# Kernel optimization log

Measured on AMD Instinct MI355X. Metric: run time of the kernel, lower is better.

Reference implementation:

```python
import jax, jax.numpy as jnp
import numpy as np

# uniform-size batching: B graphs, NC compound atoms, NP pocket residues each
B, NC, NP, H = 16, 64, 384, 128
CFEAT, PFEAT = 56, 1280
SCALE = 5.0  # coordinate_scale
LN_EPS = 1e-5


def setup_inputs() -> dict:
    key = jax.random.key(0)
    ks = jax.random.split(key, 16)
    inp = {
        "compound_feats": jax.random.normal(ks[0], (B * NC, CFEAT), jnp.float32),
        "pocket_feats": jax.random.normal(ks[1], (B * NP, PFEAT), jnp.float32),
        "complex_coords": jax.random.normal(ks[2], (B, 2 + NC + NP, 3), jnp.float32) * 10.0,
        "pocket_xyz": jax.random.normal(ks[3], (B, NP, 3), jnp.float32) * 10.0,
        "dis_map": jax.random.uniform(ks[4], (B * NP * NC,), jnp.float32) * 10.0,
        # learned parameters (xavier with gain=0.001 as in the torch init)
        "Wc": jax.random.normal(ks[5], (CFEAT, H), jnp.float32) * 0.001,
        "bc": jnp.zeros((H,), jnp.float32),
        "Wp": jax.random.normal(ks[6], (PFEAT, H), jnp.float32) * 0.001,
        "bp": jnp.zeros((H,), jnp.float32),
        "ln_g": jnp.ones((H,), jnp.float32),
        "ln_b": jnp.zeros((H,), jnp.float32),
        "W1": jax.random.normal(ks[7], (H, H), jnp.float32) * 0.001,
        "b1": jnp.zeros((H,), jnp.float32),
        "W2": jax.random.normal(ks[8], (H, 1), jnp.float32) * 0.001,
        "b2": jnp.zeros((1,), jnp.float32),
    }
    return inp


def _layernorm(x, g, b):
    m = jnp.mean(x, axis=-1, keepdims=True)
    v = jnp.mean(jnp.square(x - m), axis=-1, keepdims=True)
    return (x - m) * jax.lax.rsqrt(v + LN_EPS) * g + b


def reference(compound_feats, pocket_feats, complex_coords, pocket_xyz, dis_map,
              Wc, bc, Wp, bp, ln_g, ln_b, W1, b1, W2, b2):
    norm = lambda x: x / SCALE
    # input linears, then dense-batch (uniform sizes -> exact reshape)
    comp_emb = (compound_feats @ Wc + bc).reshape(B, NC, H)   # [B,NC,H]
    pock_emb = (pocket_feats @ Wp + bp).reshape(B, NP, H)     # [B,NP,H]
    # complex layout per graph: [glb_c, compound (NC), glb_p, pocket (NP)]
    # complex_binding_model treated as identity (see notes): emb/coords pass through.
    comp_coords_out = norm(complex_coords[:, 1:1 + NC])       # [B,NC,3] (normalized)
    pock_coords = norm(pocket_xyz)                            # [B,NP,3]
    # torch.cdist(pocket, compound): [B,NP,NC]
    diff = pock_coords[:, :, None, :] - comp_coords_out[:, None, :, :]
    pc_dis = jnp.sqrt(jnp.sum(jnp.square(diff), axis=-1))
    # layernorm + pairwise outer product + distmap MLP
    p_ln = _layernorm(pock_emb, ln_g, ln_b)
    c_ln = _layernorm(comp_emb, ln_g, ln_b)
    z = jnp.einsum('bik,bjk->bijk', p_ln, c_ln)               # [B,NP,NC,H]
    h = jax.nn.relu(z @ W1 + b1)
    b_logit = (h @ W2 + b2)[..., 0]                            # [B,NP,NC]
    # uniform sizes -> all-true masks, boolean-select is a flatten
    dis_map_pred_by_pair = jax.nn.sigmoid(b_logit.reshape(-1)) * 10.0
    dis_map_pred_by_coord = jnp.clip(pc_dis.reshape(-1) * SCALE, 0.0, 10.0)
    compound_coord_pred = (comp_coords_out * SCALE).reshape(B * NC, 3)
    compound_batch = jnp.repeat(jnp.arange(B, dtype=jnp.int32), NC)
    return (compound_coord_pred, compound_batch, dis_map_pred_by_pair,
            dis_map_pred_by_coord, dis_map)
```

## Files before the change

### kernel.cpp

```cpp
#include <hip/hip_runtime.h>
#include <hip/hip_bf16.h>

#define BB 16
#define NC 64
#define NP 384
#define HH 128
#define CF 56
#define PFT 1280

typedef float f32x4 __attribute__((ext_vector_type(4)));
typedef __bf16 bf16x8 __attribute__((ext_vector_type(8)));
typedef unsigned short u16x8 __attribute__((ext_vector_type(8)));
typedef unsigned short u16x4 __attribute__((ext_vector_type(4)));

static __device__ __forceinline__ unsigned short f2bfu(float f){
  __bf16 h = (__bf16)f;
  return __builtin_bit_cast(unsigned short, h);
}
static __device__ __forceinline__ float bfu2f(unsigned short u){
  __bf16 h = __builtin_bit_cast(__bf16, u);
  return (float)h;
}

__global__ __launch_bounds__(256) void k_prep(
    const float* __restrict__ cf, const float* __restrict__ Wc,
    const float* __restrict__ bc, const float* __restrict__ lng,
    const float* __restrict__ lnb, const float* __restrict__ Wp,
    const float* __restrict__ W1, const float* __restrict__ cc,
    const float* __restrict__ px, const float* __restrict__ dm,
    unsigned short* __restrict__ c_ln, unsigned short* __restrict__ wpt,
    unsigned short* __restrict__ w1t,
    float* __restrict__ out1, float* __restrict__ out4, float* __restrict__ out5){
  __shared__ unsigned short t[128][72];
  __shared__ float redc[2][2], redc2[2][2];
  int bx = blockIdx.x;
  int tid = threadIdx.x;
  if (bx < 20){
    int k0 = bx*64;
    #pragma unroll
    for (int i=0;i<8;i++){
      int fi = tid + i*256;
      int k  = fi>>5;
      int c4 = (fi&31)*4;
      float4 v = *(const float4*)(Wp + (size_t)(k0+k)*HH + c4);
      t[c4+0][k]=f2bfu(v.x); t[c4+1][k]=f2bfu(v.y);
      t[c4+2][k]=f2bfu(v.z); t[c4+3][k]=f2bfu(v.w);
    }
    __syncthreads();
    #pragma unroll
    for (int i=0;i<4;i++){
      int ci = tid + i*256;
      int col = ci>>3, kb = ci&7;
      u16x8 v = *(const u16x8*)&t[col][kb*8];
      *(u16x8*)(wpt + (size_t)col*PFT + k0 + kb*8) = v;
    }
  } else if (bx < 84){
    int idx = (bx-20)*256+tid;
    int k = idx>>7, m = idx&127;
    w1t[m*HH+k] = f2bfu(W1[idx]);
  } else if (bx < 596){
    int rh = tid>>7, m = tid&127;
    int row = (bx-84)*2 + rh;
    const float* cr = cf + row*CF;
    float acc = bc[m];
    #pragma unroll
    for (int k=0;k<CF;k++) acc += cr[k]*Wc[k*HH+m];
    float s=acc, s2=acc*acc;
    #pragma unroll
    for (int off=1; off<64; off<<=1){ s += __shfl_xor(s,off,64); s2 += __shfl_xor(s2,off,64); }
    int wid = (tid>>6)&1;
    if ((m&63)==0){ redc[rh][wid]=s; redc2[rh][wid]=s2; }
    __syncthreads();
    float S=redc[rh][0]+redc[rh][1], S2=redc2[rh][0]+redc2[rh][1];
    float mean = S*(1.0f/HH);
    float var  = S2*(1.0f/HH) - mean*mean;
    float rs = rsqrtf(var + 1e-5f);
    c_ln[(size_t)row*HH+m] = f2bfu((acc-mean)*rs*lng[m] + lnb[m]);
  } else if (bx < 608){
    int idx = (bx-596)*256+tid;
    if (idx < BB*NC*3){
      int bb = idx/(NC*3), rem = idx%(NC*3);
      float v = cc[(size_t)bb*(2+NC+NP)*3 + 3 + rem];
      out1[idx] = (v/5.0f)*5.0f;
    }
    if (idx < BB*NC) out1[BB*NC*3+idx] = (float)(idx>>6);
  } else {
    int idx = (bx-608)*256+tid;
    int b = idx/(NP*NC), r = idx%(NP*NC), i = r>>6, j = r&63;
    const float* pp = px + ((size_t)b*NP+i)*3;
    const float* cp = cc + (size_t)b*(2+NC+NP)*3 + 3 + (size_t)j*3;
    float dx=pp[0]/5.0f-cp[0]/5.0f;
    float dy=pp[1]/5.0f-cp[1]/5.0f;
    float dz=pp[2]/5.0f-cp[2]/5.0f;
    float d = sqrtf(dx*dx+dy*dy+dz*dz)*5.0f;
    d = fminf(fmaxf(d,0.f),10.f);
    out4[idx]=d;
    out5[idx]=dm[idx];
  }
}

__global__ __launch_bounds__(256) void k_main(
    const float* __restrict__ pf, const unsigned short* __restrict__ wpt,
    const float* __restrict__ bp, const float* __restrict__ lng,
    const float* __restrict__ lnb,
    const unsigned short* __restrict__ c_ln, const unsigned short* __restrict__ w1t,
    const float* __restrict__ b1, const float* __restrict__ W2,
    const float* __restrict__ b2p, float* __restrict__ out3){
  __shared__ __align__(16) unsigned short sA[2][16*64];
  __shared__ __align__(16) unsigned short sB[2][HH*64];
  __shared__ __align__(16) float sPf[12*HH];
  int tid = threadIdx.x;
  int w = tid>>6, lane = tid&63, q = lane&15, gr = lane>>4;
  int bx = blockIdx.x;
  int b  = bx>>5;
  int i0 = (bx&31)*12;
  size_t prow0 = (size_t)(b*NP + i0);
  *(unsigned short*)((char*)&sA[0][0] + 1536 + tid*2) = 0;
  *(unsigned short*)((char*)&sA[1][0] + 1536 + tid*2) = 0;
  f32x4 acc2[2];
  acc2[0]=(f32x4){0.f,0.f,0.f,0.f}; acc2[1]=(f32x4){0.f,0.f,0.f,0.f};
  int arow = tid>>4, ak4 = (tid&15)*4;
  float4 ra; u16x8 rb[4];
  #define LOADS1(KS) {                                                         \
    int kbase = (KS)*64;                                                       \
    if (arow < 12)                                                             \
      ra = *(const float4*)(pf + (prow0+arow)*PFT + kbase + ak4);              \
    _Pragma("unroll")                                                          \
    for (int i=0;i<4;i++){                                                     \
      int bi = tid + 256*i;                                                    \
      int col = bi>>3, kb = bi&7;                                              \
      rb[i] = *(const u16x8*)(wpt + (size_t)col*PFT + kbase + kb*8);           \
    }                                                                          \
  }
  #define WRITES1(BUF) {                                                       \
    char* A = (char*)&sA[BUF][0];                                              \
    char* Bc = (char*)&sB[BUF][0];                                             \
    if (arow < 12){                                                            \
      u16x4 h = { f2bfu(ra.x), f2bfu(ra.y), f2bfu(ra.z), f2bfu(ra.w) };        \
      *(u16x4*)(A + arow*128 + (((ak4>>3)^(arow&7))<<4) + ((ak4&7)<<1)) = h;   \
    }                                                                          \
    _Pragma("unroll")                                                          \
    for (int i=0;i<4;i++){                                                     \
      int bi = tid + 256*i;                                                    \
      int col = bi>>3, kb = bi&7;                                              \
      *(u16x8*)(Bc + col*128 + ((kb^(col&7))<<4)) = rb[i];                     \
    }                                                                          \
  }
  LOADS1(0)
  WRITES1(0)
  int cur = 0;
  for (int ks=0; ks<20; ks++){
    if (ks<19) LOADS1(ks+1)
    __syncthreads();
    char* A = (char*)&sA[cur][0];
    char* Bc = (char*)&sB[cur][0];
    #pragma unroll
    for (int kk=0;kk<2;kk++){
      bf16x8 a = *(bf16x8*)(A + q*128 + (((kk*4+gr)^(q&7))<<4));
      #pragma unroll
      for (int ct=0;ct<2;ct++){
        int col = w*32 + ct*16 + q;
        bf16x8 bfr = *(bf16x8*)(Bc + col*128 + (((kk*4+gr)^(col&7))<<4));
        acc2[ct] = __builtin_amdgcn_mfma_f32_16x16x32_bf16(a,bfr,acc2[ct],0,0,0);
      }
    }
    if (ks<19){ WRITES1(cur^1) cur ^= 1; }
  }
  __syncthreads();
  #pragma unroll
  for (int ct=0;ct<2;ct++){
    int col = w*32 + ct*16 + q;
    float bpv = bp[col];
    #pragma unroll
    for (int r=0;r<4;r++){
      int row = gr*4+r;
      if (row < 12) sPf[row*HH + col] = acc2[ct][r] + bpv;
    }
  }
  int jh = w&1, mh = w>>1;
  int j0 = jh*32, m0 = mh*64;
  u16x8 cfrag[2][4];
  #pragma unroll
  for (int jt=0;jt<2;jt++){
    const unsigned short* cb = c_ln + ((size_t)b*NC + j0 + jt*16 + q)*HH + gr*8;
    #pragma unroll
    for (int kt=0;kt<4;kt++) cfrag[jt][kt] = *(const u16x8*)(cb + kt*32);
  }
  u16x8 w1f[4][4];
  #pragma unroll
  for (int kt=0;kt<4;kt++)
    #pragma unroll
    for (int nt=0;nt<4;nt++)
      w1f[kt][nt] = *(const u16x8*)(w1t + (size_t)(m0+nt*16+q)*HH + kt*32 + gr*8);
  float b1v[4], w2v[4];
  #pragma unroll
  for (int nt=0;nt<4;nt++){ b1v[nt]=b1[m0+nt*16+q]; w2v[nt]=W2[m0+nt*16+q]; }
  float b2 = b2p[0];
  float* psumh = (float*)&sB[0][0];
  __syncthreads();
  {
    float g0 = lng[lane], g1 = lng[lane+64];
    float B0 = lnb[lane], B1 = lnb[lane+64];
    #pragma unroll
    for (int rr=0; rr<3; rr++){
      int row = w*3+rr;
      float a0 = sPf[row*HH + lane], a1 = sPf[row*HH + lane + 64];
      float s = a0+a1, s2 = a0*a0 + a1*a1;
      #pragma unroll
      for (int off=1; off<64; off<<=1){ s += __shfl_xor(s,off,64); s2 += __shfl_xor(s2,off,64); }
      float mean = s*(1.0f/HH);
      float var  = s2*(1.0f/HH) - mean*mean;
      float rs   = rsqrtf(var + 1e-5f);
      sPf[row*HH + lane]      = (a0-mean)*rs*g0 + B0;
      sPf[row*HH + lane + 64] = (a1-mean)*rs*g1 + B1;
    }
  }
  __syncthreads();
  for (int ii=0; ii<12; ii++){
    f32x4 acc[2][4];
    #pragma unroll
    for (int jt=0;jt<2;jt++)
      #pragma unroll
      for (int nt=0;nt<4;nt++) acc[jt][nt]=(f32x4){0.f,0.f,0.f,0.f};
    #pragma unroll
    for (int kt=0;kt<4;kt++){
      int kblk = kt*4+gr;
      f32x4 p0 = *(const f32x4*)&sPf[ii*HH + kblk*8];
      f32x4 p1 = *(const f32x4*)&sPf[ii*HH + kblk*8 + 4];
      #pragma unroll
      for (int jt=0;jt<2;jt++){
        u16x8 cfv = cfrag[jt][kt];
        bf16x8 a;
        #pragma unroll
        for (int e=0;e<4;e++) a[e]   = (__bf16)(bfu2f(cfv[e])*p0[e]);
        #pragma unroll
        for (int e=0;e<4;e++) a[e+4] = (__bf16)(bfu2f(cfv[e+4])*p1[e]);
        #pragma unroll
        for (int nt=0;nt<4;nt++)
          acc[jt][nt] = __builtin_amdgcn_mfma_f32_16x16x32_bf16(
              a, __builtin_bit_cast(bf16x8, w1f[kt][nt]), acc[jt][nt], 0,0,0);
      }
    }
    #pragma unroll
    for (int jt=0;jt<2;jt++){
      float part[4]={0.f,0.f,0.f,0.f};
      #pragma unroll
      for (int nt=0;nt<4;nt++)
        #pragma unroll
        for (int r=0;r<4;r++){
          float h = acc[jt][nt][r] + b1v[nt];
          h = fmaxf(h, 0.f);
          part[r] += h*w2v[nt];
        }
      #pragma unroll
      for (int r=0;r<4;r++){
        part[r]+=__shfl_xor(part[r],1,16);
        part[r]+=__shfl_xor(part[r],2,16);
        part[r]+=__shfl_xor(part[r],4,16);
        part[r]+=__shfl_xor(part[r],8,16);
      }
      if (q==0){
        #pragma unroll
        for (int r=0;r<4;r++)
          psumh[(mh*12 + ii)*64 + j0 + jt*16 + gr*4 + r] = part[r];
      }
    }
  }
  __syncthreads();
  for (int v=tid; v<12*64; v+=256){
    int ii = v>>6, j = v&63;
    float s = psumh[(0*12+ii)*64 + j] + psumh[(1*12+ii)*64 + j] + b2;
    out3[(prow0+ii)*NC + j] = 10.f/(1.f+expf(-s));
  }
}

extern "C" void kernel_launch(void* const* d_in, const int* in_sizes, int n_in,
                              void* d_out, int out_size, void* d_ws, size_t ws_size,
                              hipStream_t stream){
  const float* cf = (const float*)d_in[0];
  const float* pf = (const float*)d_in[1];
  const float* cc = (const float*)d_in[2];
  const float* px = (const float*)d_in[3];
  const float* dm = (const float*)d_in[4];
  const float* Wc = (const float*)d_in[5];
  const float* bc = (const float*)d_in[6];
  const float* Wp = (const float*)d_in[7];
  const float* bp = (const float*)d_in[8];
  const float* lng= (const float*)d_in[9];
  const float* lnb= (const float*)d_in[10];
  const float* W1 = (const float*)d_in[11];
  const float* b1 = (const float*)d_in[12];
  const float* W2 = (const float*)d_in[13];
  const float* b2 = (const float*)d_in[14];

  float* out = (float*)d_out;
  char* ws = (char*)d_ws;
  unsigned short* c_ln = (unsigned short*)ws;
  unsigned short* w1t  = (unsigned short*)(ws + 262144 + 1572864);
  unsigned short* wpt  = (unsigned short*)(ws + 262144 + 1572864 + 32768);

  float* out1 = out;
  float* out3 = out + BB*NC*3 + BB*NC;
  float* out4 = out3 + BB*NP*NC;
  float* out5 = out4 + BB*NP*NC;

  hipLaunchKernelGGL(k_prep, dim3(2144), dim3(256), 0, stream,
                     cf, Wc, bc, lng, lnb, Wp, W1, cc, px, dm,
                     c_ln, wpt, w1t, out1, out4, out5);
  hipLaunchKernelGGL(k_main, dim3(512), dim3(256), 0, stream,
                     pf, wpt, bp, lng, lnb, c_ln, w1t, b1, W2, b2, out3);
}
```

Measured before the change: 45.45 us.

## Double k_main block size with split-K projection and row-split pair MLP

k_main now runs 512 threads per block. The pocket projection is split along K across two half-blocks, which each own one of the two former double-buffer slots, and the partial sums are combined through shared memory. The pair-MLP stage splits the 12 pocket rows across two wave groups, and W1 is staged in swizzled shared memory instead of being held in registers per wave. This raises parallelism and cuts register pressure, but it removes the double buffering in the projection loop, adds extra barriers, and turns W1 register reads into LDS reads.

```diff
diff --git a/kernel.cpp b/kernel.cpp
--- a/kernel.cpp
+++ b/kernel.cpp
@@ -99,7 +99,7 @@
   }
 }
 
-__global__ __launch_bounds__(256) void k_main(
+__global__ __launch_bounds__(512) void k_main(
     const float* __restrict__ pf, const unsigned short* __restrict__ wpt,
     const float* __restrict__ bp, const float* __restrict__ lng,
     const float* __restrict__ lnb,
@@ -109,75 +109,78 @@
   __shared__ __align__(16) unsigned short sA[2][16*64];
   __shared__ __align__(16) unsigned short sB[2][HH*64];
   __shared__ __align__(16) float sPf[12*HH];
+  __shared__ __align__(16) float uComb[12*HH];
   int tid = threadIdx.x;
   int w = tid>>6, lane = tid&63, q = lane&15, gr = lane>>4;
+  int half = tid>>8, th = tid&255, wh = w&3;
   int bx = blockIdx.x;
   int b  = bx>>5;
   int i0 = (bx&31)*12;
   size_t prow0 = (size_t)(b*NP + i0);
-  *(unsigned short*)((char*)&sA[0][0] + 1536 + tid*2) = 0;
-  *(unsigned short*)((char*)&sA[1][0] + 1536 + tid*2) = 0;
+  *(unsigned short*)((char*)&sA[half][0] + 1536 + th*2) = 0;
   f32x4 acc2[2];
   acc2[0]=(f32x4){0.f,0.f,0.f,0.f}; acc2[1]=(f32x4){0.f,0.f,0.f,0.f};
-  int arow = tid>>4, ak4 = (tid&15)*4;
+  int khalf0 = half*640;
+  int arow = th>>4, ak4 = (th&15)*4;
   float4 ra; u16x8 rb[4];
   #define LOADS1(KS) {                                                         \
-    int kbase = (KS)*64;                                                       \
+    int kbase = khalf0 + (KS)*64;                                              \
     if (arow < 12)                                                             \
       ra = *(const float4*)(pf + (prow0+arow)*PFT + kbase + ak4);              \
     _Pragma("unroll")                                                          \
     for (int i=0;i<4;i++){                                                     \
-      int bi = tid + 256*i;                                                    \
+      int bi = th + 256*i;                                                     \
       int col = bi>>3, kb = bi&7;                                              \
       rb[i] = *(const u16x8*)(wpt + (size_t)col*PFT + kbase + kb*8);           \
     }                                                                          \
   }
-  #define WRITES1(BUF) {                                                       \
-    char* A = (char*)&sA[BUF][0];                                              \
-    char* Bc = (char*)&sB[BUF][0];                                             \
+  #define WRITES1() {                                                         \
+    char* A = (char*)&sA[half][0];                                             \
+    char* Bc = (char*)&sB[half][0];                                            \
     if (arow < 12){                                                            \
       u16x4 h = { f2bfu(ra.x), f2bfu(ra.y), f2bfu(ra.z), f2bfu(ra.w) };        \
       *(u16x4*)(A + arow*128 + (((ak4>>3)^(arow&7))<<4) + ((ak4&7)<<1)) = h;   \
     }                                                                          \
     _Pragma("unroll")                                                          \
     for (int i=0;i<4;i++){                                                     \
-      int bi = tid + 256*i;                                                    \
+      int bi = th + 256*i;                                                     \
       int col = bi>>3, kb = bi&7;                                              \
       *(u16x8*)(Bc + col*128 + ((kb^(col&7))<<4)) = rb[i];                     \
     }                                                                          \
   }
   LOADS1(0)
-  WRITES1(0)
-  int cur = 0;
-  for (int ks=0; ks<20; ks++){
-    if (ks<19) LOADS1(ks+1)
-    __syncthreads();
-    char* A = (char*)&sA[cur][0];
-    char* Bc = (char*)&sB[cur][0];
+  WRITES1()
+  __syncthreads();
+  for (int ks=0; ks<10; ks++){
+    if (ks<9) LOADS1(ks+1)
+    char* A = (char*)&sA[half][0];
+    char* Bc = (char*)&sB[half][0];
     #pragma unroll
     for (int kk=0;kk<2;kk++){
       bf16x8 a = *(bf16x8*)(A + q*128 + (((kk*4+gr)^(q&7))<<4));
       #pragma unroll
       for (int ct=0;ct<2;ct++){
-        int col = w*32 + ct*16 + q;
+        int col = wh*32 + ct*16 + q;
         bf16x8 bfr = *(bf16x8*)(Bc + col*128 + (((kk*4+gr)^(col&7))<<4));
         acc2[ct] = __builtin_amdgcn_mfma_f32_16x16x32_bf16(a,bfr,acc2[ct],0,0,0);
       }
     }
-    if (ks<19){ WRITES1(cur^1) cur ^= 1; }
-  }
-  __syncthreads();
-  #pragma unroll
-  for (int ct=0;ct<2;ct++){
-    int col = w*32 + ct*16 + q;
-    float bpv = bp[col];
-    #pragma unroll
-    for (int r=0;r<4;r++){
-      int row = gr*4+r;
-      if (row < 12) sPf[row*HH + col] = acc2[ct][r] + bpv;
-    }
-  }
-  int jh = w&1, mh = w>>1;
+    __syncthreads();
+    if (ks<9){ WRITES1() __syncthreads(); }
+  }
+  float* comb = uComb;
+  if (half==1){
+    #pragma unroll
+    for (int ct=0;ct<2;ct++){
+      int col = wh*32 + ct*16 + q;
+      #pragma unroll
+      for (int r=0;r<4;r++){
+        int row = gr*4+r;
+        if (row < 12) comb[row*HH + col] = acc2[ct][r];
+      }
+    }
+  }
+  int jh = w&1, mh = (w>>1)&1, ih = w>>2;
   int j0 = jh*32, m0 = mh*64;
   u16x8 cfrag[2][4];
   #pragma unroll
@@ -186,24 +189,41 @@
     #pragma unroll
     for (int kt=0;kt<4;kt++) cfrag[jt][kt] = *(const u16x8*)(cb + kt*32);
   }
-  u16x8 w1f[4][4];
-  #pragma unroll
-  for (int kt=0;kt<4;kt++)
-    #pragma unroll
-    for (int nt=0;nt<4;nt++)
-      w1f[kt][nt] = *(const u16x8*)(w1t + (size_t)(m0+nt*16+q)*HH + kt*32 + gr*8);
   float b1v[4], w2v[4];
   #pragma unroll
   for (int nt=0;nt<4;nt++){ b1v[nt]=b1[m0+nt*16+q]; w2v[nt]=W2[m0+nt*16+q]; }
   float b2 = b2p[0];
-  float* psumh = (float*)&sB[0][0];
-  __syncthreads();
+  __syncthreads();
+  if (half==0){
+    #pragma unroll
+    for (int ct=0;ct<2;ct++){
+      int col = wh*32 + ct*16 + q;
+      float bpv = bp[col];
+      #pragma unroll
+      for (int r=0;r<4;r++){
+        int row = gr*4+r;
+        if (row < 12) sPf[row*HH + col] = acc2[ct][r] + comb[row*HH + col] + bpv;
+      }
+    }
+  }
+  __syncthreads();
+  unsigned short* sW = &sB[0][0];
   {
+    const int4* srcW = (const int4*)w1t;
+    #pragma unroll
+    for (int i=0;i<4;i++){
+      int c = tid + 512*i;
+      int mm = c>>4, kb = c&15;
+      ((int4*)sW)[mm*16 + (kb^(mm&7))] = srcW[c];
+    }
+  }
+  {
+    int nr = (w<4)?2:1;
+    int r0 = (w<4)? w*2 : (w+4);
     float g0 = lng[lane], g1 = lng[lane+64];
     float B0 = lnb[lane], B1 = lnb[lane+64];
-    #pragma unroll
-    for (int rr=0; rr<3; rr++){
-      int row = w*3+rr;
+    for (int rr=0; rr<nr; rr++){
+      int row = r0+rr;
       float a0 = sPf[row*HH + lane], a1 = sPf[row*HH + lane + 64];
       float s = a0+a1, s2 = a0*a0 + a1*a1;
       #pragma unroll
@@ -216,7 +236,9 @@
     }
   }
   __syncthreads();
-  for (int ii=0; ii<12; ii++){
+  float* psumh = uComb;
+  for (int iq=0; iq<6; iq++){
+    int ii = ih*6 + iq;
     f32x4 acc[2][4];
     #pragma unroll
     for (int jt=0;jt<2;jt++)
@@ -236,9 +258,11 @@
         #pragma unroll
         for (int e=0;e<4;e++) a[e+4] = (__bf16)(bfu2f(cfv[e+4])*p1[e]);
         #pragma unroll
-        for (int nt=0;nt<4;nt++)
-          acc[jt][nt] = __builtin_amdgcn_mfma_f32_16x16x32_bf16(
-              a, __builtin_bit_cast(bf16x8, w1f[kt][nt]), acc[jt][nt], 0,0,0);
+        for (int nt=0;nt<4;nt++){
+          int mm = m0 + nt*16 + q;
+          bf16x8 bv = *(const bf16x8*)&sW[mm*HH + ((kblk^(mm&7))<<3)];
+          acc[jt][nt] = __builtin_amdgcn_mfma_f32_16x16x32_bf16(a, bv, acc[jt][nt], 0,0,0);
+        }
       }
     }
     #pragma unroll
@@ -267,9 +291,9 @@
     }
   }
   __syncthreads();
-  for (int v=tid; v<12*64; v+=256){
+  for (int v=tid; v<12*64; v+=512){
     int ii = v>>6, j = v&63;
-    float s = psumh[(0*12+ii)*64 + j] + psumh[(1*12+ii)*64 + j] + b2;
+    float s = psumh[ii*64 + j] + psumh[(12+ii)*64 + j] + b2;
     out3[(prow0+ii)*NC + j] = 10.f/(1.f+expf(-s));
   }
 }
@@ -307,6 +331,6 @@
   hipLaunchKernelGGL(k_prep, dim3(2144), dim3(256), 0, stream,
                      cf, Wc, bc, lng, lnb, Wp, W1, cc, px, dm,
                      c_ln, wpt, w1t, out1, out4, out5);
-  hipLaunchKernelGGL(k_main, dim3(512), dim3(256), 0, stream,
+  hipLaunchKernelGGL(k_main, dim3(512), dim3(512), 0, stream,
                      pf, wpt, bp, lng, lnb, c_ln, w1t, b1, W2, b2, out3);
 }
```

Measured after the change: 53.09 us. 1.17x slower.
